# Kernel optimization log

Hardware: AMD Instinct MI355X
Metric: run time of the kernel (lower is better)

The kernel has to match this reference:

```python
import math
import jax, jax.numpy as jnp
from jax import lax
import numpy as np

DN = ('NCHW', 'OIHW', 'NCHW')


def setup_inputs() -> dict:
    key = jax.random.key(0)
    k0, k1, k2, k3, k4, k5 = jax.random.split(key, 6)
    n, c, h, w = 16, 256, 64, 64
    x = jax.random.normal(k0, (n, c, h, w), jnp.float32)
    b1 = math.sqrt(3.0 / h)
    p1 = jax.random.uniform(k1, (h, c // 8), jnp.float32, -b1, b1)          # p_1_w
    p3 = jax.random.normal(k2, (c, 1, 9, 9), jnp.float32) * 0.05            # depthwise conv, groups=c
    p4 = jax.random.normal(k3, (c, 4, 5, 1), jnp.float32) * 0.05            # grouped conv, groups=c//4
    b5 = math.sqrt(3.0 / (c * w // 8))
    p5 = jax.random.uniform(k4, (c // 8, w, 1, 3 * c), jnp.float32, -b5, b5)  # p_5_w
    p6 = jax.random.normal(k5, (c, 1, 1, 3), jnp.float32) * 0.3             # depthwise conv, groups=c
    return {"x": x, "p1": p1, "p3": p3, "p4": p4, "p5": p5, "p6": p6}


def reference(x, p1, p3, p4, p5, p6):
    n, c, h, w = x.shape
    # t_1: einsum 'abcd,ce->abed' contracts h -> (n, c, c//8, w)
    t1 = jnp.einsum('nchw,he->ncew', x, p1)
    # t_2: unfold(x, (3,1), padding=(1,0)) -> (n, c, 3, h, w)
    xp = jnp.pad(x, ((0, 0), (0, 0), (1, 1), (0, 0)))
    t2 = jnp.stack([xp[:, :, k:k + h, :] for k in range(3)], axis=2)
    # p_3: 9x9 depthwise conv over the (c//8, w) 'spatial' map
    t3 = lax.conv_general_dilated(t1, p3, (1, 1), ((4, 4), (4, 4)),
                                  dimension_numbers=DN, feature_group_count=c)
    # p_4: (5,1) conv with groups=c//4
    t4 = lax.conv_general_dilated(t3, p4, (1, 1), ((2, 2), (0, 0)),
                                  dimension_numbers=DN, feature_group_count=c // 4)
    # t_5: einsum 'abcd,cdef->abef' -> (n, c, 1, 3c) -> (n, c, 3c)
    t5 = jnp.einsum('ncew,ewf->ncf', t4, p5[:, :, 0, :])
    # p_6: (1,3) depthwise conv on (n, c, 1, 3c)
    t6 = lax.conv_general_dilated(t5[:, :, None, :], p6, (1, 1), ((0, 0), (1, 1)),
                                  dimension_numbers=DN, feature_group_count=c)[:, :, 0, :]
    # scaled bmm: (n,c,3c) @ (n,3c,h*w) / sqrt(3c)
    out = jnp.einsum('ncf,nfp->ncp', t6, t2.reshape(n, 3 * c, h * w))
    return (out / math.sqrt(3 * c)).reshape(n, c, h, w)
```

## Files before the change

### kernel.cpp

```cpp
#include <hip/hip_runtime.h>

#define NB 16
#define C  256
#define H  64
#define W  64
#define E  32
#define F  768
#define HW 4096
#define K5 2048
#define XROWS 4224

typedef __attribute__((ext_vector_type(2))) float f32x2;
typedef __attribute__((ext_vector_type(4))) float f32x4;
typedef __attribute__((ext_vector_type(16))) float f32x16;
typedef __attribute__((ext_vector_type(8))) short s16x8;

__device__ inline unsigned short to_bf16(float f) {
  union { float f; unsigned u; } v; v.f = f;
  unsigned u = v.u;
  u += 0x7fff + ((u >> 16) & 1);
  return (unsigned short)(u >> 16);
}

__device__ inline float from_bf16(unsigned short s) {
  union { unsigned u; float f; } v; v.u = ((unsigned)s) << 16;
  return v.f;
}

__device__ inline void gload16(const void* g, void* l) {
  __builtin_amdgcn_global_load_lds((const __attribute__((address_space(1))) unsigned int*)g,
                                   (__attribute__((address_space(3))) unsigned int*)l, 16, 0, 0);
}

__global__ __launch_bounds__(256) void k_prep(const float* __restrict__ p5,
                                              unsigned short* __restrict__ p5t,
                                              const float* __restrict__ p3,
                                              float* __restrict__ w3p) {
  const int bid = blockIdx.x;
  const int tid = threadIdx.x;
  if (bid < 384) {
    const int f0 = (bid % 12) * 64;
    const int k0 = (bid / 12) * 64;
    __shared__ __align__(16) unsigned short ls[64][264];
    int fl = tid & 63, k4 = tid >> 6;
    for (int i = 0; i < 16; ++i) {
      int kl = k4 * 16 + i;
      ls[fl][kl] = to_bf16(p5[(size_t)(k0 + kl) * F + f0 + fl]);
    }
    __syncthreads();
#pragma unroll
    for (int j = 0; j < 2; ++j) {
      int chunk = tid + 256 * j;
      int row = chunk >> 3, slot = chunk & 7;
      *(uint4*)(p5t + (size_t)(f0 + row) * K5 + k0 + slot * 8) = *(const uint4*)&ls[row][slot * 8];
    }
  } else {
    const int c = bid - 384;
    if (tid >= 180) return;
    const int i = tid / 20, s = tid % 20;
    const float* wr = p3 + c * 81 + i * 9;
    float v;
    if (s < 10) {
      int q = s >> 1, e = s & 1;
      v = (q < 4) ? wr[2 * q + e] : (e ? 0.f : wr[8]);
    } else {
      int s2 = s - 10, q = s2 >> 1, e = s2 & 1;
      v = (q == 0) ? (e ? wr[0] : 0.f) : wr[2 * (q - 1) + 1 + e];
    }
    w3p[(size_t)(c * 9 + i) * 20 + s] = v;
  }
}

__global__ __launch_bounds__(256) void k_t13(const float* __restrict__ x,
                                             const float* __restrict__ p1,
                                             const float* __restrict__ w3p,
                                             unsigned short* __restrict__ t3g) {
  const int nc = blockIdx.x;
  const int c = nc & 255;
  const int tid = threadIdx.x;
  const int lane = tid & 63;
  const int wv = tid >> 6;

  __shared__ __align__(16) unsigned short xs[64][64];
  __shared__ __align__(16) float t1s[40][76];

  for (int i = tid; i < 40 * 76; i += 256) (&t1s[0][0])[i] = 0.f;

  s16x8 afr[2][2];
  {
    const int r = lane & 15;
    const int kb = (lane >> 4) * 8;
#pragma unroll
    for (int m = 0; m < 2; ++m)
#pragma unroll
      for (int kc = 0; kc < 2; ++kc) {
        s16x8 tmp;
#pragma unroll
        for (int j = 0; j < 8; ++j)
          tmp[j] = (short)to_bf16(p1[(kc * 32 + kb + j) * 32 + m * 16 + r]);
        afr[m][kc] = tmp;
      }
  }
  {
    const float* xp = x + (size_t)nc * HW;
#pragma unroll
    for (int t = 0; t < 2; ++t) {
      int uid = tid + 256 * t;
      int h = uid >> 3, uc = uid & 7;
      float4 v0 = *(const float4*)(xp + h * 64 + uc * 8);
      float4 v1 = *(const float4*)(xp + h * 64 + uc * 8 + 4);
      unsigned short b[8] = {to_bf16(v0.x), to_bf16(v0.y), to_bf16(v0.z), to_bf16(v0.w),
                             to_bf16(v1.x), to_bf16(v1.y), to_bf16(v1.z), to_bf16(v1.w)};
      *(uint4*)((char*)&xs[0][0] + h * 128 + ((uc ^ ((h >> 3) & 7)) * 16)) = *(const uint4*)b;
    }
  }
  __syncthreads();
  {
    const int wcol = wv * 16 + (lane & 15);
    f32x4 cf[2] = {{0.f, 0.f, 0.f, 0.f}, {0.f, 0.f, 0.f, 0.f}};
#pragma unroll
    for (int kc = 0; kc < 2; ++kc) {
      const int kb = kc * 32 + (lane >> 4) * 8;
      const char* base = (const char*)&xs[0][0] +
                         kb * 128 + (((wcol >> 3) ^ ((kb >> 3) & 7)) * 16) + (wcol & 7) * 2;
      s16x8 bfrag;
#pragma unroll
      for (int j = 0; j < 8; ++j)
        bfrag[j] = *(const short*)(base + j * 128);
      cf[0] = __builtin_amdgcn_mfma_f32_16x16x32_bf16(afr[0][kc], bfrag, cf[0], 0, 0, 0);
      cf[1] = __builtin_amdgcn_mfma_f32_16x16x32_bf16(afr[1][kc], bfrag, cf[1], 0, 0, 0);
    }
#pragma unroll
    for (int m = 0; m < 2; ++m)
#pragma unroll
      for (int q = 0; q < 4; ++q)
        t1s[4 + m * 16 + (lane >> 4) * 4 + q][4 + wcol] = cf[m][q];
  }
  __syncthreads();
  unsigned short* plane = t3g + (size_t)nc * 2304;
  if (tid < 32) {
    static const int zr[4] = {0, 1, 34, 35};
    int row = zr[tid >> 3], col = (tid & 7) * 8;
    uint4 z = make_uint4(0, 0, 0, 0);
    *(uint4*)(plane + row * 64 + col) = z;
  }
  const int e = tid >> 3, w0 = (tid & 7) * 8;
  f32x2 opk[8] = {};
#pragma unroll
  for (int i = 0; i < 9; ++i) {
    const float* r = &t1s[e + i][w0];
    f32x4 v0 = *(const f32x4*)(r);
    f32x4 v1 = *(const f32x4*)(r + 4);
    f32x4 v2 = *(const f32x4*)(r + 8);
    f32x4 v3 = *(const f32x4*)(r + 12);
    f32x2 wa[8];
    wa[0] = __builtin_shufflevector(v0, v0, 0, 1);
    wa[1] = __builtin_shufflevector(v0, v0, 2, 3);
    wa[2] = __builtin_shufflevector(v1, v1, 0, 1);
    wa[3] = __builtin_shufflevector(v1, v1, 2, 3);
    wa[4] = __builtin_shufflevector(v2, v2, 0, 1);
    wa[5] = __builtin_shufflevector(v2, v2, 2, 3);
    wa[6] = __builtin_shufflevector(v3, v3, 0, 1);
    wa[7] = __builtin_shufflevector(v3, v3, 2, 3);
    const f32x2* wp = (const f32x2*)(w3p + (size_t)(c * 9 + i) * 20);
    f32x2 we0 = wp[0], we1 = wp[1], we2 = wp[2], we3 = wp[3], we4 = wp[4];
    f32x2 wo0 = wp[5], wo1 = wp[6], wo2 = wp[7], wo3 = wp[8], wo4 = wp[9];
#pragma unroll
    for (int t = 0; t < 4; ++t) {
      f32x2 aE = opk[2 * t], aO = opk[2 * t + 1];
      aE += wa[t] * we0;
      aE += wa[t + 1] * we1;
      aE += wa[t + 2] * we2;
      aE += wa[t + 3] * we3;
      aE += wa[t + 4] * we4;
      aO += wa[t] * wo0;
      aO += wa[t + 1] * wo1;
      aO += wa[t + 2] * wo2;
      aO += wa[t + 3] * wo3;
      aO += wa[t + 4] * wo4;
      opk[2 * t] = aE;
      opk[2 * t + 1] = aO;
    }
  }
  unsigned short ob[8];
#pragma unroll
  for (int k = 0; k < 8; ++k) ob[k] = to_bf16(opk[k].x + opk[k].y);
  *(uint4*)(plane + (2 + e) * 64 + w0) = *(const uint4*)ob;
}

__global__ __launch_bounds__(256) void k_t4kg(const unsigned short* __restrict__ t3g,
                                              const float* __restrict__ p4,
                                              unsigned short* __restrict__ t4b) {
  const int blk = blockIdx.x;
  const int c0 = (blk & 63) * 4;
  const int n = blk >> 6;
  const int tid = threadIdx.x;
  __shared__ __align__(16) unsigned short t3s[4 * 36 * 64];

  const unsigned short* src = t3g + ((size_t)(n * C + c0)) * 2304;
  for (int i = tid; i < 1152; i += 256) {
    int rf = i >> 3, sl = i & 7;
    int sw = sl ^ (rf & 7);
    gload16((const char*)src + rf * 128 + sw * 16, (char*)t3s + i * 16);
  }
  __syncthreads();

  const int e = tid >> 3, w0q = tid & 7;
  float acc[4][8];
#pragma unroll
  for (int qo = 0; qo < 4; ++qo)
#pragma unroll
    for (int k = 0; k < 8; ++k) acc[qo][k] = 0.f;
#pragma unroll
  for (int ci = 0; ci < 4; ++ci) {
#pragma unroll
    for (int u = 0; u < 5; ++u) {
      int rf = ci * 36 + e + u;
      uint4 v = *(const uint4*)((const char*)t3s + rf * 128 + ((w0q ^ (rf & 7)) * 16));
      const unsigned short* vs = (const unsigned short*)&v;
      float vf[8];
#pragma unroll
      for (int k = 0; k < 8; ++k) vf[k] = from_bf16(vs[k]);
#pragma unroll
      for (int qo = 0; qo < 4; ++qo) {
        float wv = p4[(c0 + qo) * 20 + ci * 5 + u];
#pragma unroll
        for (int k = 0; k < 8; ++k) acc[qo][k] += vf[k] * wv;
      }
    }
  }
#pragma unroll
  for (int qo = 0; qo < 4; ++qo) {
    unsigned short ob[8];
#pragma unroll
    for (int k = 0; k < 8; ++k) ob[k] = to_bf16(acc[qo][k]);
    *(uint4*)(t4b + ((size_t)(n * C + c0 + qo)) * 2048 + e * 64 + w0q * 8) = *(const uint4*)ob;
  }
}

__global__ __launch_bounds__(256) void k_xt(const float* __restrict__ x,
                                            unsigned short* __restrict__ xt) {
  const int hi = blockIdx.x;
  const int n = blockIdx.y;
  const int tid = threadIdx.x;
  unsigned short* dst = xt + ((size_t)n * XROWS + hi * 64) * C;
  if (hi == 0 || hi == 65) {
    uint4 z = make_uint4(0, 0, 0, 0);
    uint4* d4 = (uint4*)dst;
#pragma unroll
    for (int i = 0; i < 8; ++i) d4[tid + 256 * i] = z;
    return;
  }
  const int h = hi - 1;
  __shared__ __align__(16) unsigned short ls[64][264];
  const float* xp = x + ((size_t)n * C) * HW + h * 64;
  int w = tid & 63, c4 = tid >> 6;
  for (int i = 0; i < 64; ++i) {
    int c = c4 * 64 + i;
    ls[w][c] = to_bf16(xp[(size_t)c * HW + w]);
  }
  __syncthreads();
#pragma unroll
  for (int j = 0; j < 8; ++j) {
    int chunk = tid + 256 * j;
    int row = chunk >> 5, slot = chunk & 31;
    *(uint4*)(dst + row * C + slot * 8) = *(const uint4*)&ls[row][slot * 8];
  }
}

__global__ __launch_bounds__(256) void k_t5m(const unsigned short* __restrict__ A,
                                             const unsigned short* __restrict__ Bt,
                                             unsigned short* __restrict__ Cout) {
  const int bid = blockIdx.x;
  const int wg = (bid & 7) * 96 + (bid >> 3);
  const int nt = wg % 12;
  const int mt = wg / 12;
  const int n0 = nt * 64;
  const int m0 = mt * 64;
  const int tid = threadIdx.x;
  const int lane = tid & 63;
  const int wave = tid >> 6;
  const int wm = wave >> 1, wn = wave & 1;
  __shared__ __align__(16) short As[8192];
  __shared__ __align__(16) short Bs[8192];
  f32x16 acc = {};

  for (int k0 = 0; k0 < K5; k0 += 128) {
#pragma unroll
    for (int i = 0; i < 4; ++i) {
      int chunk = i * 256 + tid;
      int r = chunk >> 4, sl = chunk & 15;
      int sw = sl ^ (r & 15);
      gload16((const char*)(A + (size_t)(m0 + r) * K5 + k0) + sw * 16,
              (char*)As + chunk * 16);
      gload16((const char*)(Bt + (size_t)(n0 + r) * K5 + k0) + sw * 16,
              (char*)Bs + chunk * 16);
    }
    __syncthreads();
#pragma unroll
    for (int kq = 0; kq < 8; ++kq) {
      int arow = wm * 32 + (lane & 31);
      int aslot = (kq * 2 + (lane >> 5)) ^ (arow & 15);
      s16x8 af = *(const s16x8*)((const char*)As + arow * 256 + aslot * 16);
      int brow = wn * 32 + (lane & 31);
      int bslot = (kq * 2 + (lane >> 5)) ^ (brow & 15);
      s16x8 bf = *(const s16x8*)((const char*)Bs + brow * 256 + bslot * 16);
      acc = __builtin_amdgcn_mfma_f32_32x32x16_bf16(af, bf, acc, 0, 0, 0);
    }
    __syncthreads();
  }
  const int col = n0 + wn * 32 + (lane & 31);
#pragma unroll
  for (int r = 0; r < 16; ++r) {
    int grow = m0 + wm * 32 + (r & 3) + 8 * (r >> 2) + 4 * (lane >> 5);
    Cout[(size_t)grow * F + col] = to_bf16(acc[r]);
  }
}

__global__ __launch_bounds__(256) void k_t6(const unsigned short* __restrict__ t5b,
                                            const float* __restrict__ p6,
                                            unsigned short* __restrict__ t6b) {
  int idx = blockIdx.x * 256 + threadIdx.x;
  if (idx >= NB * C * F) return;
  int fp = idx % F;
  int nc = idx / F;
  int c = nc & 255;
  int c2 = fp & 255;
  int kk = fp >> 8;
  int f = 3 * c2 + kk;
  const unsigned short* row = t5b + (size_t)nc * F;
  const float* wt = p6 + c * 3;
  float acc = from_bf16(row[f]) * wt[1];
  if (f > 0) acc += from_bf16(row[f - 1]) * wt[0];
  if (f < F - 1) acc += from_bf16(row[f + 1]) * wt[2];
  t6b[idx] = to_bf16(acc * 0.03608439182435161f);
}

__global__ __launch_bounds__(512, 4) void k_outm(const unsigned short* __restrict__ t6b,
                                                 const unsigned short* __restrict__ xt,
                                                 float* __restrict__ outp) {
  const int bid = blockIdx.x;
  const int wg = (bid & 7) * 64 + (bid >> 3);
  const int n  = wg >> 5;
  const int tile = wg & 31;
  const int p0 = (tile & 15) * 256;
  const int m0 = (tile >> 4) * 128;
  const int tid = threadIdx.x;
  const int lane = tid & 63;
  const int wid = tid >> 6;
  const int wm = wid >> 2;
  const int wn = wid & 3;
  __shared__ __align__(16) short As[8192];
  __shared__ __align__(16) short Bs[16384];
  f32x16 acc[2][2] = {};
  const unsigned short* Abase = t6b + (size_t)(n * C) * F + m0 * F;
  const unsigned short* Xbase = xt + (size_t)n * XROWS * C;

  for (int kt = 0; kt < 12; ++kt) {
    const int k0 = kt * 64;
    const int kk = k0 >> 8, c20 = k0 & 255;
#pragma unroll
    for (int i = 0; i < 2; ++i) {
      int chunk = i * 512 + tid;
      int r = chunk >> 3, sl = chunk & 7, sw = sl ^ (r & 7);
      gload16((const char*)(Abase + (size_t)r * F + k0) + sw * 16,
              (char*)As + chunk * 16);
    }
#pragma unroll
    for (int i = 0; i < 4; ++i) {
      int chunk = i * 512 + tid;
      int r = chunk >> 3, sl = chunk & 7, sw = sl ^ (r & 7);
      gload16((const char*)(Xbase + (size_t)(p0 + r + (kk << 6)) * C + c20) + sw * 16,
              (char*)Bs + chunk * 16);
    }
    __syncthreads();
#pragma unroll
    for (int kq = 0; kq < 4; ++kq) {
      s16x8 af[2], bf[2];
#pragma unroll
      for (int mi = 0; mi < 2; ++mi) {
        int row = wm * 64 + mi * 32 + (lane & 31);
        int byte = (row * 128 + kq * 32 + ((lane >> 5) * 16)) ^ ((row & 7) << 4);
        af[mi] = *(const s16x8*)((const char*)As + byte);
      }
#pragma unroll
      for (int ni = 0; ni < 2; ++ni) {
        int row = wn * 64 + ni * 32 + (lane & 31);
        int byte = (row * 128 + kq * 32 + ((lane >> 5) * 16)) ^ ((row & 7) << 4);
        bf[ni] = *(const s16x8*)((const char*)Bs + byte);
      }
#pragma unroll
      for (int mi = 0; mi < 2; ++mi)
#pragma unroll
        for (int ni = 0; ni < 2; ++ni)
          acc[mi][ni] = __builtin_amdgcn_mfma_f32_32x32x16_bf16(af[mi], bf[ni], acc[mi][ni], 0, 0, 0);
    }
    __syncthreads();
  }
  float* obase = outp + ((size_t)(n * C) + m0) * HW;
#pragma unroll
  for (int mi = 0; mi < 2; ++mi) {
#pragma unroll
    for (int ni = 0; ni < 2; ++ni) {
      int gcol = p0 + wn * 64 + ni * 32 + (lane & 31);
#pragma unroll
      for (int r = 0; r < 16; ++r) {
        int grow = wm * 64 + mi * 32 + (r & 3) + 8 * (r >> 2) + 4 * (lane >> 5);
        obase[(size_t)grow * HW + gcol] = acc[mi][ni][r];
      }
    }
  }
}

extern "C" void kernel_launch(void* const* d_in, const int* in_sizes, int n_in,
                              void* d_out, int out_size, void* d_ws, size_t ws_size,
                              hipStream_t stream) {
  (void)in_sizes; (void)n_in; (void)out_size; (void)ws_size;
  const float* x  = (const float*)d_in[0];
  const float* p1 = (const float*)d_in[1];
  const float* p3 = (const float*)d_in[2];
  const float* p4 = (const float*)d_in[3];
  const float* p5 = (const float*)d_in[4];
  const float* p6 = (const float*)d_in[5];
  float* out = (float*)d_out;

  char* ws = (char*)d_ws;
  unsigned short* t3g = (unsigned short*)ws;
  unsigned short* t4b = (unsigned short*)(ws + 18874368);
  unsigned short* p5t = (unsigned short*)(ws + 35651584);
  unsigned short* t5b = (unsigned short*)(ws + 38797312);
  float*          w3p = (float*)(ws + 47290368);
  unsigned short* t6b = (unsigned short*)ws;
  unsigned short* xt  = (unsigned short*)(ws + 6291456);

  k_prep<<<dim3(640), 256, 0, stream>>>(p5, p5t, p3, w3p);
  k_t13 <<<dim3(NB * C), 256, 0, stream>>>(x, p1, w3p, t3g);
  k_t4kg<<<dim3(NB * 64), 256, 0, stream>>>(t3g, p4, t4b);
  k_t5m <<<dim3(768), 256, 0, stream>>>(t4b, p5t, t5b);
  k_t6  <<<dim3((NB * C * F + 255) / 256), 256, 0, stream>>>(t5b, p6, t6b);
  k_xt  <<<dim3(66, NB), 256, 0, stream>>>(x, xt);
  k_outm<<<dim3(512), 512, 0, stream>>>(t6b, xt, out);
}
```

Measured before the change: 121.5 us.

## Fold prep kernel into t13 launch and retile t5 GEMM to 128x128

The separate prep kernel is removed. The p5 transpose runs as extra blocks appended to the k_t13 grid, and each t13 block now builds its own repacked 9x9 weights in shared memory instead of reading them from global. This saves one kernel launch and the global round trip for the weights. Separately, the t5 GEMM moves from 64x64 tiles with 256 threads to 128x128 tiles with 512 threads and a K-step of 64, so each wave computes two MFMA tiles and operands get more reuse. In exchange, the GEMM launches only 192 blocks, which may underfill the GPU's compute units.

```diff
diff --git a/kernel.cpp b/kernel.cpp
--- a/kernel.cpp
+++ b/kernel.cpp
@@ -32,17 +32,23 @@
                                    (__attribute__((address_space(3))) unsigned int*)l, 16, 0, 0);
 }
 
-__global__ __launch_bounds__(256) void k_prep(const float* __restrict__ p5,
-                                              unsigned short* __restrict__ p5t,
-                                              const float* __restrict__ p3,
-                                              float* __restrict__ w3p) {
+__global__ __launch_bounds__(256) void k_t13(const float* __restrict__ x,
+                                             const float* __restrict__ p1,
+                                             const float* __restrict__ p3,
+                                             const float* __restrict__ p5,
+                                             unsigned short* __restrict__ p5t,
+                                             unsigned short* __restrict__ t3g) {
+  __shared__ __align__(16) char smem[21088];
+  const int tid = threadIdx.x;
   const int bid = blockIdx.x;
-  const int tid = threadIdx.x;
-  if (bid < 384) {
-    const int f0 = (bid % 12) * 64;
-    const int k0 = (bid / 12) * 64;
-    __shared__ __align__(16) unsigned short ls[64][264];
-    int fl = tid & 63, k4 = tid >> 6;
+
+  if (bid >= NB * C) {
+    unsigned short (*ls)[72] = (unsigned short(*)[72])smem;
+    const int tb = bid - NB * C;
+    const int f0 = (tb % 12) * 64;
+    const int k0 = (tb / 12) * 64;
+    const int fl = tid & 63, k4 = tid >> 6;
+#pragma unroll
     for (int i = 0; i < 16; ++i) {
       int kl = k4 * 16 + i;
       ls[fl][kl] = to_bf16(p5[(size_t)(k0 + kl) * F + f0 + fl]);
@@ -54,9 +60,20 @@
       int row = chunk >> 3, slot = chunk & 7;
       *(uint4*)(p5t + (size_t)(f0 + row) * K5 + k0 + slot * 8) = *(const uint4*)&ls[row][slot * 8];
     }
-  } else {
-    const int c = bid - 384;
-    if (tid >= 180) return;
+    return;
+  }
+
+  unsigned short (*xs)[64] = (unsigned short(*)[64])smem;
+  float (*t1s)[76] = (float(*)[76])(smem + 8192);
+  float* w3s = (float*)(smem + 20352);
+
+  const int nc = bid;
+  const int c = nc & 255;
+  const int lane = tid & 63;
+  const int wv = tid >> 6;
+
+  for (int i = tid; i < 40 * 76; i += 256) (&t1s[0][0])[i] = 0.f;
+  if (tid < 180) {
     const int i = tid / 20, s = tid % 20;
     const float* wr = p3 + c * 81 + i * 9;
     float v;
@@ -67,24 +84,8 @@
       int s2 = s - 10, q = s2 >> 1, e = s2 & 1;
       v = (q == 0) ? (e ? wr[0] : 0.f) : wr[2 * (q - 1) + 1 + e];
     }
-    w3p[(size_t)(c * 9 + i) * 20 + s] = v;
-  }
-}
-
-__global__ __launch_bounds__(256) void k_t13(const float* __restrict__ x,
-                                             const float* __restrict__ p1,
-                                             const float* __restrict__ w3p,
-                                             unsigned short* __restrict__ t3g) {
-  const int nc = blockIdx.x;
-  const int c = nc & 255;
-  const int tid = threadIdx.x;
-  const int lane = tid & 63;
-  const int wv = tid >> 6;
-
-  __shared__ __align__(16) unsigned short xs[64][64];
-  __shared__ __align__(16) float t1s[40][76];
-
-  for (int i = tid; i < 40 * 76; i += 256) (&t1s[0][0])[i] = 0.f;
+    w3s[i * 20 + s] = v;
+  }
 
   s16x8 afr[2][2];
   {
@@ -162,7 +163,7 @@
     wa[5] = __builtin_shufflevector(v2, v2, 2, 3);
     wa[6] = __builtin_shufflevector(v3, v3, 0, 1);
     wa[7] = __builtin_shufflevector(v3, v3, 2, 3);
-    const f32x2* wp = (const f32x2*)(w3p + (size_t)(c * 9 + i) * 20);
+    const f32x2* wp = (const f32x2*)(w3s + i * 20);
     f32x2 we0 = wp[0], we1 = wp[1], we2 = wp[2], we3 = wp[3], we4 = wp[4];
     f32x2 wo0 = wp[5], wo1 = wp[6], wo2 = wp[7], wo3 = wp[8], wo4 = wp[9];
 #pragma unroll
@@ -268,29 +269,30 @@
   }
 }
 
-__global__ __launch_bounds__(256) void k_t5m(const unsigned short* __restrict__ A,
-                                             const unsigned short* __restrict__ Bt,
-                                             unsigned short* __restrict__ Cout) {
+__global__ __launch_bounds__(512, 4) void k_t5m(const unsigned short* __restrict__ A,
+                                                const unsigned short* __restrict__ Bt,
+                                                unsigned short* __restrict__ Cout) {
   const int bid = blockIdx.x;
-  const int wg = (bid & 7) * 96 + (bid >> 3);
-  const int nt = wg % 12;
-  const int mt = wg / 12;
-  const int n0 = nt * 64;
-  const int m0 = mt * 64;
+  const int wg = (bid & 7) * 24 + (bid >> 3);
+  const int nt = wg % 6;
+  const int mt = wg / 6;
+  const int n0 = nt * 128;
+  const int m0 = mt * 128;
   const int tid = threadIdx.x;
   const int lane = tid & 63;
-  const int wave = tid >> 6;
-  const int wm = wave >> 1, wn = wave & 1;
+  const int wid = tid >> 6;
+  const int wm = wid >> 2;
+  const int wn = wid & 3;
   __shared__ __align__(16) short As[8192];
   __shared__ __align__(16) short Bs[8192];
-  f32x16 acc = {};
-
-  for (int k0 = 0; k0 < K5; k0 += 128) {
-#pragma unroll
-    for (int i = 0; i < 4; ++i) {
-      int chunk = i * 256 + tid;
-      int r = chunk >> 4, sl = chunk & 15;
-      int sw = sl ^ (r & 15);
+  f32x16 acc[2] = {};
+
+  for (int k0 = 0; k0 < K5; k0 += 64) {
+#pragma unroll
+    for (int i = 0; i < 2; ++i) {
+      int chunk = i * 512 + tid;
+      int r = chunk >> 3, sl = chunk & 7;
+      int sw = sl ^ (r & 7);
       gload16((const char*)(A + (size_t)(m0 + r) * K5 + k0) + sw * 16,
               (char*)As + chunk * 16);
       gload16((const char*)(Bt + (size_t)(n0 + r) * K5 + k0) + sw * 16,
@@ -298,22 +300,33 @@
     }
     __syncthreads();
 #pragma unroll
-    for (int kq = 0; kq < 8; ++kq) {
-      int arow = wm * 32 + (lane & 31);
-      int aslot = (kq * 2 + (lane >> 5)) ^ (arow & 15);
-      s16x8 af = *(const s16x8*)((const char*)As + arow * 256 + aslot * 16);
-      int brow = wn * 32 + (lane & 31);
-      int bslot = (kq * 2 + (lane >> 5)) ^ (brow & 15);
-      s16x8 bf = *(const s16x8*)((const char*)Bs + brow * 256 + bslot * 16);
-      acc = __builtin_amdgcn_mfma_f32_32x32x16_bf16(af, bf, acc, 0, 0, 0);
+    for (int kq = 0; kq < 4; ++kq) {
+      s16x8 af[2], bf;
+#pragma unroll
+      for (int mi = 0; mi < 2; ++mi) {
+        int row = wm * 64 + mi * 32 + (lane & 31);
+        int byte = (row * 128 + kq * 32 + ((lane >> 5) * 16)) ^ ((row & 7) << 4);
+        af[mi] = *(const s16x8*)((const char*)As + byte);
+      }
+      {
+        int row = wn * 32 + (lane & 31);
+        int byte = (row * 128 + kq * 32 + ((lane >> 5) * 16)) ^ ((row & 7) << 4);
+        bf = *(const s16x8*)((const char*)Bs + byte);
+      }
+#pragma unroll
+      for (int mi = 0; mi < 2; ++mi)
+        acc[mi] = __builtin_amdgcn_mfma_f32_32x32x16_bf16(af[mi], bf, acc[mi], 0, 0, 0);
     }
     __syncthreads();
   }
   const int col = n0 + wn * 32 + (lane & 31);
 #pragma unroll
-  for (int r = 0; r < 16; ++r) {
-    int grow = m0 + wm * 32 + (r & 3) + 8 * (r >> 2) + 4 * (lane >> 5);
-    Cout[(size_t)grow * F + col] = to_bf16(acc[r]);
+  for (int mi = 0; mi < 2; ++mi) {
+#pragma unroll
+    for (int r = 0; r < 16; ++r) {
+      int grow = m0 + wm * 64 + mi * 32 + (r & 3) + 8 * (r >> 2) + 4 * (lane >> 5);
+      Cout[(size_t)grow * F + col] = to_bf16(acc[mi][r]);
+    }
   }
 }
 
@@ -429,14 +442,12 @@
   unsigned short* t4b = (unsigned short*)(ws + 18874368);
   unsigned short* p5t = (unsigned short*)(ws + 35651584);
   unsigned short* t5b = (unsigned short*)(ws + 38797312);
-  float*          w3p = (float*)(ws + 47290368);
   unsigned short* t6b = (unsigned short*)ws;
   unsigned short* xt  = (unsigned short*)(ws + 6291456);
 
-  k_prep<<<dim3(640), 256, 0, stream>>>(p5, p5t, p3, w3p);
-  k_t13 <<<dim3(NB * C), 256, 0, stream>>>(x, p1, w3p, t3g);
+  k_t13 <<<dim3(NB * C + 384), 256, 0, stream>>>(x, p1, p3, p5, p5t, t3g);
   k_t4kg<<<dim3(NB * 64), 256, 0, stream>>>(t3g, p4, t4b);
-  k_t5m <<<dim3(768), 256, 0, stream>>>(t4b, p5t, t5b);
+  k_t5m <<<dim3(192), 512, 0, stream>>>(t4b, p5t, t5b);
   k_t6  <<<dim3((NB * C * F + 255) / 256), 256, 0, stream>>>(t5b, p6, t6b);
   k_xt  <<<dim3(66, NB), 256, 0, stream>>>(x, xt);
   k_outm<<<dim3(512), 512, 0, stream>>>(t6b, xt, out);
```

Result: slower. 131.9 us (+8.6%).
